# Kernel optimization log

Hardware: AMD Instinct MI355X
Metric: run time of the kernel (lower is better)

## Reference

```python
import jax, jax.numpy as jnp
import numpy as np

BLOCK = 128
QMAX = 127.0


def _quant_dequant_act(x2d):
    """Dynamic per-token, per-128-column-group INT8 quantize + dequantize.

    x2d: [T, K]. Groups of shape 1x128 along K (is_weight=False path).
    """
    T, K = x2d.shape
    xb = x2d.reshape(T, K // BLOCK, BLOCK)
    amax = jnp.max(jnp.abs(xb), axis=-1, keepdims=True)
    scale = jnp.where(amax > 0, amax / QMAX, 1.0)
    q = jnp.clip(jnp.round(xb / scale), -QMAX, QMAX)  # int8 values
    return (q * scale).reshape(T, K)


def _quant_dequant_weight(w):
    """128x128 blockwise INT8 quantize + dequantize (is_weight=True path).

    w: [O, K] with O, K multiples of 128.
    """
    O, K = w.shape
    wb = w.reshape(O // BLOCK, BLOCK, K // BLOCK, BLOCK)
    amax = jnp.max(jnp.abs(wb), axis=(1, 3), keepdims=True)
    scale = jnp.where(amax > 0, amax / QMAX, 1.0)
    q = jnp.clip(jnp.round(wb / scale), -QMAX, QMAX)
    return (q * scale).reshape(O, K)


def setup_inputs() -> dict:
    key = jax.random.key(0)
    k1, k2, k3 = jax.random.split(key, 3)
    B, S, K, O = 4, 2048, 4096, 11008
    x = jax.random.normal(k1, (B, S, K), dtype=jnp.float32)
    w = jax.random.normal(k2, (O, K), dtype=jnp.float32) * 0.02
    bias = jax.random.normal(k3, (O,), dtype=jnp.float32) * 0.01
    return {"x": x, "w": w, "bias": bias}


def reference(x, w, bias):
    """INT8Linear forward: dynamic per-token INT8 activation quantization +
    128x128 blockwise-scaled INT8 weight GEMM + bias.

    Because scales are constant within each (token-group x weight-block),
    the blockwise-scaled int8 GEMM is mathematically identical to
    dequantize-then-matmul, which is the efficient dense expression here.
    """
    in_shape = x.shape
    x2d = x.reshape(-1, in_shape[-1])        # [T, K]
    xdq = _quant_dequant_act(x2d)            # [T, K]
    wdq = _quant_dequant_weight(w)           # [O, K]
    y = jnp.einsum('tk,ok->to', xdq, wdq) + bias
    return y.reshape(*in_shape[:-1], w.shape[0])
```

## Files before the change

kernel.cpp:

```cpp
#include <hip/hip_runtime.h>
#include <hip/hip_bf16.h>
#include <stdint.h>

#define QMAXF 127.0f

typedef __attribute__((ext_vector_type(4))) float f32x4;
typedef __attribute__((ext_vector_type(4))) int i32x4;

typedef __attribute__((address_space(1))) void gbl_void;
typedef __attribute__((address_space(3))) void lds_void;

__device__ __forceinline__ void gload_lds16(const void* g, void* l) {
    __builtin_amdgcn_global_load_lds((const gbl_void*)g, (lds_void*)l, 16, 0, 0);
}

__global__ __launch_bounds__(256) void qd_x_kernel(const float* __restrict__ x,
                                                   char* __restrict__ qx,
                                                   float* __restrict__ sxT,
                                                   long ngroups, int nkb, int T) {
    long gw = ((long)blockIdx.x * blockDim.x + threadIdx.x) >> 6;
    int lane = threadIdx.x & 63;
    if (gw >= ngroups) return;

    float2 v = *(reinterpret_cast<const float2*>(x) + gw * 64 + lane);
    float a = fmaxf(fabsf(v.x), fabsf(v.y));
#pragma unroll
    for (int off = 32; off; off >>= 1) a = fmaxf(a, __shfl_xor(a, off));

    float scale = a > 0.f ? a / QMAXF : 1.f;
    int q0 = (int)fminf(fmaxf(rintf(v.x / scale), -QMAXF), QMAXF);
    int q1 = (int)fminf(fmaxf(rintf(v.y / scale), -QMAXF), QMAXF);
    unsigned short packed = (unsigned short)((q0 & 0xFF) | ((q1 & 0xFF) << 8));
    reinterpret_cast<unsigned short*>(qx)[gw * 64 + lane] = packed;

    if (lane == 0) {
        int t = (int)(gw / nkb), kb = (int)(gw - (long)t * nkb);
        sxT[(size_t)kb * T + t] = scale;
    }
}

__global__ __launch_bounds__(256) void qd_w_kernel(const float* __restrict__ w,
                                                   char* __restrict__ qw,
                                                   float* __restrict__ sw,
                                                   int K, int nkb) {
    int kb = blockIdx.x, ob = blockIdx.y;
    size_t base = (size_t)ob * 128 * K + (size_t)kb * 128;
    int t = threadIdx.x;

    float4 v[16];
    float a = 0.f;
#pragma unroll
    for (int i = 0; i < 16; i++) {
        int f = i * 256 + t;
        int row = f >> 5, c4 = f & 31;
        v[i] = *reinterpret_cast<const float4*>(w + base + (size_t)row * K + c4 * 4);
        a = fmaxf(a, fmaxf(fmaxf(fabsf(v[i].x), fabsf(v[i].y)),
                           fmaxf(fabsf(v[i].z), fabsf(v[i].w))));
    }
#pragma unroll
    for (int off = 32; off; off >>= 1) a = fmaxf(a, __shfl_xor(a, off));

    __shared__ float red[4];
    if ((t & 63) == 0) red[t >> 6] = a;
    __syncthreads();
    a = fmaxf(fmaxf(red[0], red[1]), fmaxf(red[2], red[3]));

    float scale = a > 0.f ? a / QMAXF : 1.f;
    if (t == 0) sw[(size_t)ob * nkb + kb] = scale;
#pragma unroll
    for (int i = 0; i < 16; i++) {
        int f = i * 256 + t;
        int row = f >> 5, c4 = f & 31;
        int q0 = (int)fminf(fmaxf(rintf(v[i].x / scale), -QMAXF), QMAXF);
        int q1 = (int)fminf(fmaxf(rintf(v[i].y / scale), -QMAXF), QMAXF);
        int q2 = (int)fminf(fmaxf(rintf(v[i].z / scale), -QMAXF), QMAXF);
        int q3 = (int)fminf(fmaxf(rintf(v[i].w / scale), -QMAXF), QMAXF);
        unsigned int p = (q0 & 0xFF) | ((q1 & 0xFF) << 8) | ((q2 & 0xFF) << 16) |
                         ((unsigned int)(q3 & 0xFF) << 24);
        *reinterpret_cast<unsigned int*>(qw + base + (size_t)row * K + c4 * 4) = p;
    }
}

#define GBM 256
#define GBN 256
#define SLOT_BY 65536

#define BAR()                              \
    do {                                   \
        asm volatile("" ::: "memory");     \
        __builtin_amdgcn_s_barrier();      \
        asm volatile("" ::: "memory");     \
    } while (0)
#define WAITL0()                                          \
    do {                                                  \
        asm volatile("s_waitcnt lgkmcnt(0)" ::: "memory");\
        __builtin_amdgcn_sched_barrier(0);                \
    } while (0)
#define WAITV0() asm volatile("s_waitcnt vmcnt(0)" ::: "memory")
#define SCHED0() __builtin_amdgcn_sched_barrier(0)

__global__ __launch_bounds__(512, 2) void gemm_i8_kernel(
    const char* __restrict__ Aq,
    const char* __restrict__ Bq,
    const float* __restrict__ sxT,
    const float* __restrict__ swp,
    const float* __restrict__ bias,
    float* __restrict__ C,
    int M, int N, int K) {
    __shared__ alignas(16) unsigned char lds8[2 * SLOT_BY];

    int nTm = M / GBM, nTn = N / GBN;
    int nwg = gridDim.x, wg = blockIdx.x;
    int mt, nt;
    if ((nTm & 7) == 0 && (32 % (nTm >> 3)) == 0) {
        int x = wg & 7, j = wg >> 3;
        int mper = nTm >> 3;
        int G = 32 / mper;
        int wsz = mper * G;
        int fullw = nTn / G;
        int jfull = fullw * wsz;
        int g, r, width;
        if (j < jfull) { g = j / wsz; r = j - g * wsz; width = G; }
        else { g = fullw; r = j - jfull; width = nTn - fullw * G; }
        mt = x * mper + r / width;
        nt = g * G + r % width;
    } else {
        int swz = (nwg & 7) ? wg : ((wg & 7) * (nwg >> 3) + (wg >> 3));
        mt = swz / nTn; nt = swz - mt * nTn;
    }

    int t = threadIdx.x, wid = t >> 6, lane = t & 63;
    int wm = wid >> 2, wn = wid & 3;
    int lr = lane & 15, lq = lane >> 4;
    int nkb = K >> 7;

    const char* Abase = Aq + (size_t)mt * GBM * K;
    const char* Bbase = Bq + (size_t)nt * GBN * K;

    int cid0 = t, cid1 = 512 + t;
    int rl0 = cid0 >> 3, rl1 = cid1 >> 3;
    int pc0 = cid0 & 7, pc1 = cid1 & 7;
    int gc0 = (pc0 ^ (rl0 & 7)) * 16, gc1 = (pc1 ^ (rl1 & 7)) * 16;

    auto STAGE = [&](int slot, int mat, int half, int kb) {
        const char* gb = (mat ? Bbase : Abase) + (size_t)(half * 128) * K + kb;
        unsigned char* db = lds8 + slot * SLOT_BY + mat * 32768 + half * 16384;
        gload_lds16(gb + (size_t)rl0 * K + gc0, db + cid0 * 16);
        gload_lds16(gb + (size_t)rl1 * K + gc1, db + cid1 * 16);
    };

    int offA[4][2], offB[2][2];
#pragma unroll
    for (int m = 0; m < 4; m++) {
        int row = wm * 128 + m * 16 + lr;
#pragma unroll
        for (int kk = 0; kk < 2; kk++)
            offA[m][kk] = row * 128 + (((kk * 4 + lq) ^ (lr & 7)) << 4);
    }
#pragma unroll
    for (int n = 0; n < 2; n++) {
        int row = wn * 64 + n * 16 + lr;
#pragma unroll
        for (int kk = 0; kk < 2; kk++)
            offB[n][kk] = 32768 + row * 128 + (((kk * 4 + lq) ^ (lr & 7)) << 4);
    }

    f32x4 facc[8][4];
#pragma unroll
    for (int m = 0; m < 8; m++)
#pragma unroll
        for (int n = 0; n < 4; n++) facc[m][n] = (f32x4){0.f, 0.f, 0.f, 0.f};

    i32x4 a[4][2], b[2][2], ia[4][2];

    auto LDA = [&](int slot, int mq) {
        const unsigned char* base = lds8 + slot * SLOT_BY + mq * 8192;
#pragma unroll
        for (int m = 0; m < 4; m++)
#pragma unroll
            for (int kk = 0; kk < 2; kk++)
                a[m][kk] = *reinterpret_cast<const i32x4*>(base + offA[m][kk]);
    };
    auto LDB = [&](int slot, int nq) {
        const unsigned char* base = lds8 + slot * SLOT_BY + nq * 4096;
#pragma unroll
        for (int n = 0; n < 2; n++)
#pragma unroll
            for (int kk = 0; kk < 2; kk++)
                b[n][kk] = *reinterpret_cast<const i32x4*>(base + offB[n][kk]);
    };
    auto MMA = [&]() {
        __builtin_amdgcn_s_setprio(1);
#pragma unroll
        for (int m = 0; m < 4; m++)
#pragma unroll
            for (int n = 0; n < 2; n++) {
                ia[m][n] = __builtin_amdgcn_mfma_i32_16x16x64_i8(
                    a[m][0], b[n][0], (i32x4){0, 0, 0, 0}, 0, 0, 0);
                ia[m][n] = __builtin_amdgcn_mfma_i32_16x16x64_i8(
                    a[m][1], b[n][1], ia[m][n], 0, 0, 0);
            }
        __builtin_amdgcn_s_setprio(0);
    };
    f32x4 sx4[4];
    float sw;
    auto FIX = [&](int mq, int nq) {
#pragma unroll
        for (int m = 0; m < 4; m++) {
            f32x4 sxw = sx4[m] * sw;
#pragma unroll
            for (int n = 0; n < 2; n++) {
                f32x4 cv;
#pragma unroll
                for (int r = 0; r < 4; r++) cv[r] = (float)ia[m][n][r];
                facc[mq * 4 + m][nq * 2 + n] += cv * sxw;
            }
        }
    };
    int sxrow0 = mt * GBM + wm * 128 + lq * 4;
    auto LDSX = [&](int i, int mq) {
#pragma unroll
        for (int m = 0; m < 4; m++)
            sx4[m] = *reinterpret_cast<const f32x4*>(
                sxT + (size_t)i * M + sxrow0 + mq * 64 + m * 16);
    };

    int swbase = (nt * 2 + (wn >> 1)) * nkb;

    STAGE(0, 0, 0, 0); STAGE(0, 0, 1, 0);
    STAGE(0, 1, 0, 0); STAGE(0, 1, 1, 0);
    WAITV0();
    BAR();

    for (int i = 0; i < nkb; ++i) {
        int p = i & 1, q = p ^ 1;
        int knext = (i + 1 < nkb ? i + 1 : i) * 128;

        LDA(p, 0); LDB(p, 0);
        STAGE(q, 0, 0, knext); STAGE(q, 1, 0, knext);
        LDSX(i, 0);
        sw = swp[swbase + i];
        BAR(); WAITL0();
        MMA(); FIX(0, 0);
        BAR();
        LDB(p, 1);
        STAGE(q, 0, 1, knext); STAGE(q, 1, 1, knext);
        BAR(); WAITL0();
        MMA(); FIX(0, 1);
        BAR();
        LDA(p, 1);
        LDSX(i, 1);
        BAR(); WAITL0();
        MMA(); FIX(1, 1);
        BAR();
        LDB(p, 0);
        BAR(); WAITL0();
        MMA(); FIX(1, 0);
        WAITV0();
        BAR();
    }

    float bvv[4];
#pragma unroll
    for (int n = 0; n < 4; n++) bvv[n] = bias[nt * GBN + wn * 64 + n * 16 + lr];

#pragma unroll
    for (int m = 0; m < 8; m++) {
#pragma unroll
        for (int r = 0; r < 4; r++) {
            size_t row = (size_t)(mt * GBM + wm * 128 + m * 16 + lq * 4 + r);
            float* Crow = C + row * N + nt * GBN + wn * 64 + lr;
#pragma unroll
            for (int n = 0; n < 4; n++) Crow[n * 16] = facc[m][n][r] + bvv[n];
        }
    }
}

extern "C" void kernel_launch(void* const* d_in, const int* in_sizes, int n_in,
                              void* d_out, int out_size, void* d_ws, size_t ws_size,
                              hipStream_t stream) {
    const float* x = (const float*)d_in[0];
    const float* w = (const float*)d_in[1];
    const float* bias = (const float*)d_in[2];
    float* y = (float*)d_out;

    int O = in_sizes[2];
    int K = in_sizes[1] / O;
    int T = in_sizes[0] / K;
    int nkb = K / 128;

    char* qx = (char*)d_ws;
    size_t off = ((size_t)T * K + 255) & ~(size_t)255;
    char* qw = (char*)d_ws + off;
    off += ((size_t)O * K + 255) & ~(size_t)255;
    float* sxT = (float*)((char*)d_ws + off);
    off += ((size_t)nkb * T * 4 + 255) & ~(size_t)255;
    float* sw = (float*)((char*)d_ws + off);

    long ngroups = (long)T * nkb;
    qd_x_kernel<<<dim3((unsigned)((ngroups + 3) / 4)), dim3(256), 0, stream>>>(
        x, qx, sxT, ngroups, nkb, T);
    qd_w_kernel<<<dim3(nkb, O / 128), dim3(256), 0, stream>>>(w, qw, sw, K, nkb);

    int grid = (T / GBM) * (O / GBN);
    gemm_i8_kernel<<<dim3(grid), dim3(512), 0, stream>>>(qx, qw, sxT, sw, bias, y,
                                                         T, O, K);
}
```

Measured before the change: 703.3 us.

## Restructure int8 GEMM main loop into 3-stage ring with 64-wide K sub-tiles

Replaces the double-buffered 128-K pipeline with a three-slot LDS ring of 64-K sub-tiles, prefetching two stages ahead with partial vmcnt waits so there is one barrier per sub-step instead of many. Activation scales are now staged into LDS alongside the tiles, and the weight scales are loaded once per wave and broadcast with a shuffle instead of being read from global memory every step. Occupancy drops from 2 to 1 workgroup per CU. The integer accumulators now cover only 64 of K before each float rescale, which doubles the convert and FMA fix-up work per MFMA.

Result: slower. 809.4 us (+15.1%).

```diff
diff --git a/kernel.cpp b/kernel.cpp
--- a/kernel.cpp
+++ b/kernel.cpp
@@ -83,7 +83,12 @@
 
 #define GBM 256
 #define GBN 256
-#define SLOT_BY 65536
+#define SUBK 64
+#define A_BY 16384
+#define B_BY 16384
+#define SX_BY 1024
+#define SLOT_BY (A_BY + B_BY + SX_BY)
+#define RING 3
 
 #define BAR()                              \
     do {                                   \
@@ -96,10 +101,9 @@
         asm volatile("s_waitcnt lgkmcnt(0)" ::: "memory");\
         __builtin_amdgcn_sched_barrier(0);                \
     } while (0)
-#define WAITV0() asm volatile("s_waitcnt vmcnt(0)" ::: "memory")
-#define SCHED0() __builtin_amdgcn_sched_barrier(0)
-
-__global__ __launch_bounds__(512, 2) void gemm_i8_kernel(
+#define WAITV(n) asm volatile("s_waitcnt vmcnt(" #n ")" ::: "memory")
+
+__global__ __launch_bounds__(512, 1) void gemm_i8_kernel(
     const char* __restrict__ Aq,
     const char* __restrict__ Bq,
     const float* __restrict__ sxT,
@@ -107,7 +111,7 @@
     const float* __restrict__ bias,
     float* __restrict__ C,
     int M, int N, int K) {
-    __shared__ alignas(16) unsigned char lds8[2 * SLOT_BY];
+    __shared__ alignas(16) unsigned char lds8[RING * SLOT_BY];
 
     int nTm = M / GBM, nTn = N / GBN;
     int nwg = gridDim.x, wg = blockIdx.x;
@@ -133,37 +137,44 @@
     int wm = wid >> 2, wn = wid & 3;
     int lr = lane & 15, lq = lane >> 4;
     int nkb = K >> 7;
+    int NSUB = K / SUBK;
 
     const char* Abase = Aq + (size_t)mt * GBM * K;
     const char* Bbase = Bq + (size_t)nt * GBN * K;
 
-    int cid0 = t, cid1 = 512 + t;
-    int rl0 = cid0 >> 3, rl1 = cid1 >> 3;
-    int pc0 = cid0 & 7, pc1 = cid1 & 7;
-    int gc0 = (pc0 ^ (rl0 & 7)) * 16, gc1 = (pc1 ^ (rl1 & 7)) * 16;
-
-    auto STAGE = [&](int slot, int mat, int half, int kb) {
-        const char* gb = (mat ? Bbase : Abase) + (size_t)(half * 128) * K + kb;
-        unsigned char* db = lds8 + slot * SLOT_BY + mat * 32768 + half * 16384;
-        gload_lds16(gb + (size_t)rl0 * K + gc0, db + cid0 * 16);
-        gload_lds16(gb + (size_t)rl1 * K + gc1, db + cid1 * 16);
+    {
+    }
+    int rA0 = t >> 2;
+    int pcc = t & 3;
+    int cA0 = (pcc ^ ((rA0 >> 1) & 3)) << 4;
+    const char* gA = Abase + (size_t)rA0 * K + cA0;
+    const char* gB = Bbase + (size_t)rA0 * K + cA0;
+    const char* gSX = (const char*)sxT + ((size_t)mt * GBM + (t & 63) * 4) * 4;
+    size_t rowStep = (size_t)128 * K;
+
+    auto STAGE = [&](int slot, int j) {
+        size_t kb = (size_t)j * SUBK;
+        unsigned char* sb = lds8 + slot * SLOT_BY;
+        gload_lds16(gA + kb, sb + t * 16);
+        gload_lds16(gA + rowStep + kb, sb + (512 + t) * 16);
+        gload_lds16(gB + kb, sb + A_BY + t * 16);
+        gload_lds16(gB + rowStep + kb, sb + A_BY + (512 + t) * 16);
+        gload_lds16(gSX + (size_t)(j >> 1) * M * 4, sb + A_BY + B_BY + (t & 63) * 16);
     };
 
-    int offA[4][2], offB[2][2];
-#pragma unroll
-    for (int m = 0; m < 4; m++) {
-        int row = wm * 128 + m * 16 + lr;
-#pragma unroll
-        for (int kk = 0; kk < 2; kk++)
-            offA[m][kk] = row * 128 + (((kk * 4 + lq) ^ (lr & 7)) << 4);
-    }
-#pragma unroll
-    for (int n = 0; n < 2; n++) {
-        int row = wn * 64 + n * 16 + lr;
-#pragma unroll
-        for (int kk = 0; kk < 2; kk++)
-            offB[n][kk] = 32768 + row * 128 + (((kk * 4 + lq) ^ (lr & 7)) << 4);
-    }
+    int physXor = (lq ^ ((lr >> 1) & 3)) << 4;
+    int offA[2][4], offB[4], offSX[2][4];
+#pragma unroll
+    for (int mq = 0; mq < 2; mq++)
+#pragma unroll
+        for (int m = 0; m < 4; m++) {
+            int row = wm * 128 + mq * 64 + m * 16;
+            offA[mq][m] = (row + lr) * 64 + physXor;
+            offSX[mq][m] = A_BY + B_BY + (row + lq * 4) * 4;
+        }
+#pragma unroll
+    for (int n = 0; n < 4; n++)
+        offB[n] = A_BY + (wn * 64 + n * 16 + lr) * 64 + physXor;
 
     f32x4 facc[8][4];
 #pragma unroll
@@ -171,94 +182,63 @@
 #pragma unroll
         for (int n = 0; n < 4; n++) facc[m][n] = (f32x4){0.f, 0.f, 0.f, 0.f};
 
-    i32x4 a[4][2], b[2][2], ia[4][2];
-
-    auto LDA = [&](int slot, int mq) {
-        const unsigned char* base = lds8 + slot * SLOT_BY + mq * 8192;
-#pragma unroll
-        for (int m = 0; m < 4; m++)
-#pragma unroll
-            for (int kk = 0; kk < 2; kk++)
-                a[m][kk] = *reinterpret_cast<const i32x4*>(base + offA[m][kk]);
-    };
-    auto LDB = [&](int slot, int nq) {
-        const unsigned char* base = lds8 + slot * SLOT_BY + nq * 4096;
-#pragma unroll
-        for (int n = 0; n < 2; n++)
-#pragma unroll
-            for (int kk = 0; kk < 2; kk++)
-                b[n][kk] = *reinterpret_cast<const i32x4*>(base + offB[n][kk]);
-    };
-    auto MMA = [&]() {
-        __builtin_amdgcn_s_setprio(1);
-#pragma unroll
-        for (int m = 0; m < 4; m++)
-#pragma unroll
-            for (int n = 0; n < 2; n++) {
-                ia[m][n] = __builtin_amdgcn_mfma_i32_16x16x64_i8(
-                    a[m][0], b[n][0], (i32x4){0, 0, 0, 0}, 0, 0, 0);
-                ia[m][n] = __builtin_amdgcn_mfma_i32_16x16x64_i8(
-                    a[m][1], b[n][1], ia[m][n], 0, 0, 0);
+    float swv = (lane < nkb) ? swp[(size_t)(nt * 2 + (wn >> 1)) * nkb + lane] : 0.f;
+
+    auto COMPUTE = [&](int slot, float swq) {
+        const unsigned char* sb = lds8 + slot * SLOT_BY;
+        i32x4 b[4];
+#pragma unroll
+        for (int n = 0; n < 4; n++)
+            b[n] = *reinterpret_cast<const i32x4*>(sb + offB[n]);
+#pragma unroll
+        for (int mq = 0; mq < 2; mq++) {
+            i32x4 a[4];
+            f32x4 sx4[4];
+#pragma unroll
+            for (int m = 0; m < 4; m++)
+                a[m] = *reinterpret_cast<const i32x4*>(sb + offA[mq][m]);
+#pragma unroll
+            for (int m = 0; m < 4; m++)
+                sx4[m] = *reinterpret_cast<const f32x4*>(sb + offSX[mq][m]);
+            WAITL0();
+            __builtin_amdgcn_s_setprio(1);
+#pragma unroll
+            for (int nq = 0; nq < 2; nq++) {
+                i32x4 ia[4][2];
+#pragma unroll
+                for (int m = 0; m < 4; m++)
+#pragma unroll
+                    for (int n2 = 0; n2 < 2; n2++)
+                        ia[m][n2] = __builtin_amdgcn_mfma_i32_16x16x64_i8(
+                            a[m], b[nq * 2 + n2], (i32x4){0, 0, 0, 0}, 0, 0, 0);
+#pragma unroll
+                for (int m = 0; m < 4; m++) {
+                    f32x4 s = sx4[m] * swq;
+#pragma unroll
+                    for (int n2 = 0; n2 < 2; n2++) {
+                        f32x4 cv;
+#pragma unroll
+                        for (int r = 0; r < 4; r++) cv[r] = (float)ia[m][n2][r];
+                        facc[mq * 4 + m][nq * 2 + n2] += cv * s;
+                    }
+                }
             }
-        __builtin_amdgcn_s_setprio(0);
-    };
-    f32x4 sx4[4];
-    float sw;
-    auto FIX = [&](int mq, int nq) {
-#pragma unroll
-        for (int m = 0; m < 4; m++) {
-            f32x4 sxw = sx4[m] * sw;
-#pragma unroll
-            for (int n = 0; n < 2; n++) {
-                f32x4 cv;
-#pragma unroll
-                for (int r = 0; r < 4; r++) cv[r] = (float)ia[m][n][r];
-                facc[mq * 4 + m][nq * 2 + n] += cv * sxw;
-            }
+            __builtin_amdgcn_s_setprio(0);
         }
     };
-    int sxrow0 = mt * GBM + wm * 128 + lq * 4;
-    auto LDSX = [&](int i, int mq) {
-#pragma unroll
-        for (int m = 0; m < 4; m++)
-            sx4[m] = *reinterpret_cast<const f32x4*>(
-                sxT + (size_t)i * M + sxrow0 + mq * 64 + m * 16);
-    };
-
-    int swbase = (nt * 2 + (wn >> 1)) * nkb;
-
-    STAGE(0, 0, 0, 0); STAGE(0, 0, 1, 0);
-    STAGE(0, 1, 0, 0); STAGE(0, 1, 1, 0);
-    WAITV0();
-    BAR();
-
-    for (int i = 0; i < nkb; ++i) {
-        int p = i & 1, q = p ^ 1;
-        int knext = (i + 1 < nkb ? i + 1 : i) * 128;
-
-        LDA(p, 0); LDB(p, 0);
-        STAGE(q, 0, 0, knext); STAGE(q, 1, 0, knext);
-        LDSX(i, 0);
-        sw = swp[swbase + i];
-        BAR(); WAITL0();
-        MMA(); FIX(0, 0);
+
+    STAGE(0, 0);
+    STAGE(1, 1);
+
+    for (int j = 0; j < NSUB; ++j) {
+        WAITV(5);
         BAR();
-        LDB(p, 1);
-        STAGE(q, 0, 1, knext); STAGE(q, 1, 1, knext);
-        BAR(); WAITL0();
-        MMA(); FIX(0, 1);
-        BAR();
-        LDA(p, 1);
-        LDSX(i, 1);
-        BAR(); WAITL0();
-        MMA(); FIX(1, 1);
-        BAR();
-        LDB(p, 0);
-        BAR(); WAITL0();
-        MMA(); FIX(1, 0);
-        WAITV0();
-        BAR();
-    }
+        int jn = j + 2 > NSUB - 1 ? NSUB - 1 : j + 2;
+        STAGE((j + 2) % RING, jn);
+        float swq = __shfl(swv, j >> 1);
+        COMPUTE(j % RING, swq);
+    }
+    asm volatile("s_waitcnt vmcnt(0)" ::: "memory");
 
     float bvv[4];
 #pragma unroll
```

## Restructure int8 GEMM main loop into two M-halves with fewer barriers

Applied to the files above, without the earlier changes.

The per-k-block loop moves from four quarter phases, each with its own barriers and partial LDS loads, to two M-half phases. Each phase loads all of B once and issues the full 4x4 MFMA set with the scale fix-up done inline. The next tile's global-to-LDS staging is issued at the top of the iteration, followed by targeted vmcnt waits and one barrier per iteration. Launch bounds drop to one workgroup per CU to allow more registers, so occupancy falls and latency hiding rests on the in-loop overlap.

After: 746.3 us. 1.06x slower.

```diff
diff --git a/kernel.cpp b/kernel.cpp
--- a/kernel.cpp
+++ b/kernel.cpp
@@ -96,10 +96,10 @@
         asm volatile("s_waitcnt lgkmcnt(0)" ::: "memory");\
         __builtin_amdgcn_sched_barrier(0);                \
     } while (0)
-#define WAITV0() asm volatile("s_waitcnt vmcnt(0)" ::: "memory")
+#define WAITV(n) asm volatile("s_waitcnt vmcnt(" #n ")" ::: "memory")
 #define SCHED0() __builtin_amdgcn_sched_barrier(0)
 
-__global__ __launch_bounds__(512, 2) void gemm_i8_kernel(
+__global__ __launch_bounds__(512, 1) void gemm_i8_kernel(
     const char* __restrict__ Aq,
     const char* __restrict__ Bq,
     const float* __restrict__ sxT,
@@ -109,12 +109,12 @@
     int M, int N, int K) {
     __shared__ alignas(16) unsigned char lds8[2 * SLOT_BY];
 
-    int nTm = M / GBM, nTn = N / GBN;
+    int nTm = M >> 8, nTn = N >> 8;
     int nwg = gridDim.x, wg = blockIdx.x;
     int mt, nt;
-    if ((nTm & 7) == 0 && (32 % (nTm >> 3)) == 0) {
+    int mper = nTm >> 3;
+    if ((nTm & 7) == 0 && mper > 0 && (32 % mper) == 0) {
         int x = wg & 7, j = wg >> 3;
-        int mper = nTm >> 3;
         int G = 32 / mper;
         int wsz = mper * G;
         int fullw = nTn / G;
@@ -139,17 +139,24 @@
 
     int cid0 = t, cid1 = 512 + t;
     int rl0 = cid0 >> 3, rl1 = cid1 >> 3;
-    int pc0 = cid0 & 7, pc1 = cid1 & 7;
-    int gc0 = (pc0 ^ (rl0 & 7)) * 16, gc1 = (pc1 ^ (rl1 & 7)) * 16;
-
-    auto STAGE = [&](int slot, int mat, int half, int kb) {
-        const char* gb = (mat ? Bbase : Abase) + (size_t)(half * 128) * K + kb;
-        unsigned char* db = lds8 + slot * SLOT_BY + mat * 32768 + half * 16384;
-        gload_lds16(gb + (size_t)rl0 * K + gc0, db + cid0 * 16);
-        gload_lds16(gb + (size_t)rl1 * K + gc1, db + cid1 * 16);
-    };
-
-    int offA[4][2], offB[2][2];
+    int gc0 = ((cid0 & 7) ^ (rl0 & 7)) * 16, gc1 = ((cid1 & 7) ^ (rl1 & 7)) * 16;
+
+    auto STAGE8 = [&](int slot, int kb) {
+        unsigned char* sb = lds8 + slot * SLOT_BY;
+#pragma unroll
+        for (int half = 0; half < 2; half++) {
+            const char* ga = Abase + (size_t)(half * 128) * K + kb;
+            const char* gb = Bbase + (size_t)(half * 128) * K + kb;
+            unsigned char* da = sb + half * 16384;
+            unsigned char* db = sb + 32768 + half * 16384;
+            gload_lds16(ga + (size_t)rl0 * K + gc0, da + cid0 * 16);
+            gload_lds16(ga + (size_t)rl1 * K + gc1, da + cid1 * 16);
+            gload_lds16(gb + (size_t)rl0 * K + gc0, db + cid0 * 16);
+            gload_lds16(gb + (size_t)rl1 * K + gc1, db + cid1 * 16);
+        }
+    };
+
+    int offA[4][2], offB[4][2];
 #pragma unroll
     for (int m = 0; m < 4; m++) {
         int row = wm * 128 + m * 16 + lr;
@@ -158,7 +165,7 @@
             offA[m][kk] = row * 128 + (((kk * 4 + lq) ^ (lr & 7)) << 4);
     }
 #pragma unroll
-    for (int n = 0; n < 2; n++) {
+    for (int n = 0; n < 4; n++) {
         int row = wn * 64 + n * 16 + lr;
 #pragma unroll
         for (int kk = 0; kk < 2; kk++)
@@ -171,7 +178,9 @@
 #pragma unroll
         for (int n = 0; n < 4; n++) facc[m][n] = (f32x4){0.f, 0.f, 0.f, 0.f};
 
-    i32x4 a[4][2], b[2][2], ia[4][2];
+    i32x4 aH[4][2], b[4][2];
+    f32x4 sx4[4];
+    float swq = 0.f;
 
     auto LDA = [&](int slot, int mq) {
         const unsigned char* base = lds8 + slot * SLOT_BY + mq * 8192;
@@ -179,43 +188,15 @@
         for (int m = 0; m < 4; m++)
 #pragma unroll
             for (int kk = 0; kk < 2; kk++)
-                a[m][kk] = *reinterpret_cast<const i32x4*>(base + offA[m][kk]);
-    };
-    auto LDB = [&](int slot, int nq) {
-        const unsigned char* base = lds8 + slot * SLOT_BY + nq * 4096;
-#pragma unroll
-        for (int n = 0; n < 2; n++)
+                aH[m][kk] = *reinterpret_cast<const i32x4*>(base + offA[m][kk]);
+    };
+    auto LDB = [&](int slot) {
+        const unsigned char* base = lds8 + slot * SLOT_BY;
+#pragma unroll
+        for (int n = 0; n < 4; n++)
 #pragma unroll
             for (int kk = 0; kk < 2; kk++)
                 b[n][kk] = *reinterpret_cast<const i32x4*>(base + offB[n][kk]);
-    };
-    auto MMA = [&]() {
-        __builtin_amdgcn_s_setprio(1);
-#pragma unroll
-        for (int m = 0; m < 4; m++)
-#pragma unroll
-            for (int n = 0; n < 2; n++) {
-                ia[m][n] = __builtin_amdgcn_mfma_i32_16x16x64_i8(
-                    a[m][0], b[n][0], (i32x4){0, 0, 0, 0}, 0, 0, 0);
-                ia[m][n] = __builtin_amdgcn_mfma_i32_16x16x64_i8(
-                    a[m][1], b[n][1], ia[m][n], 0, 0, 0);
-            }
-        __builtin_amdgcn_s_setprio(0);
-    };
-    f32x4 sx4[4];
-    float sw;
-    auto FIX = [&](int mq, int nq) {
-#pragma unroll
-        for (int m = 0; m < 4; m++) {
-            f32x4 sxw = sx4[m] * sw;
-#pragma unroll
-            for (int n = 0; n < 2; n++) {
-                f32x4 cv;
-#pragma unroll
-                for (int r = 0; r < 4; r++) cv[r] = (float)ia[m][n][r];
-                facc[mq * 4 + m][nq * 2 + n] += cv * sxw;
-            }
-        }
     };
     int sxrow0 = mt * GBM + wm * 128 + lq * 4;
     auto LDSX = [&](int i, int mq) {
@@ -224,39 +205,54 @@
             sx4[m] = *reinterpret_cast<const f32x4*>(
                 sxT + (size_t)i * M + sxrow0 + mq * 64 + m * 16);
     };
+    auto MQ = [&](int mq) {
+        __builtin_amdgcn_s_setprio(1);
+#pragma unroll
+        for (int m = 0; m < 4; m++) {
+            i32x4 ia[4];
+#pragma unroll
+            for (int n = 0; n < 4; n++) {
+                ia[n] = __builtin_amdgcn_mfma_i32_16x16x64_i8(aH[m][0], b[n][0],
+                                                              (i32x4){0, 0, 0, 0}, 0, 0, 0);
+                ia[n] = __builtin_amdgcn_mfma_i32_16x16x64_i8(aH[m][1], b[n][1],
+                                                              ia[n], 0, 0, 0);
+            }
+            f32x4 s = sx4[m] * swq;
+#pragma unroll
+            for (int n = 0; n < 4; n++) {
+#pragma unroll
+                for (int r = 0; r < 4; r++)
+                    facc[mq * 4 + m][n][r] += (float)ia[n][r] * s[r];
+            }
+        }
+        __builtin_amdgcn_s_setprio(0);
+    };
 
     int swbase = (nt * 2 + (wn >> 1)) * nkb;
 
-    STAGE(0, 0, 0, 0); STAGE(0, 0, 1, 0);
-    STAGE(0, 1, 0, 0); STAGE(0, 1, 1, 0);
-    WAITV0();
+    STAGE8(0, 0);
+    WAITV(0);
     BAR();
 
     for (int i = 0; i < nkb; ++i) {
         int p = i & 1, q = p ^ 1;
         int knext = (i + 1 < nkb ? i + 1 : i) * 128;
 
-        LDA(p, 0); LDB(p, 0);
-        STAGE(q, 0, 0, knext); STAGE(q, 1, 0, knext);
         LDSX(i, 0);
-        sw = swp[swbase + i];
-        BAR(); WAITL0();
-        MMA(); FIX(0, 0);
-        BAR();
-        LDB(p, 1);
-        STAGE(q, 0, 1, knext); STAGE(q, 1, 1, knext);
-        BAR(); WAITL0();
-        MMA(); FIX(0, 1);
-        BAR();
+        swq = swp[swbase + i];
+        SCHED0();
+        STAGE8(q, knext);
+        SCHED0();
+        LDA(p, 0);
+        LDB(p);
+        WAITL0();
+        WAITV(8);
+        MQ(0);
         LDA(p, 1);
         LDSX(i, 1);
-        BAR(); WAITL0();
-        MMA(); FIX(1, 1);
-        BAR();
-        LDB(p, 0);
-        BAR(); WAITL0();
-        MMA(); FIX(1, 0);
-        WAITV0();
+        WAITL0();
+        WAITV(0);
+        MQ(1);
         BAR();
     }
 
@@ -302,7 +298,7 @@
         x, qx, sxT, ngroups, nkb, T);
     qd_w_kernel<<<dim3(nkb, O / 128), dim3(256), 0, stream>>>(w, qw, sw, K, nkb);
 
-    int grid = (T / GBM) * (O / GBN);
+    int grid = (T / 256) * (O / 256);
     gemm_i8_kernel<<<dim3(grid), dim3(512), 0, stream>>>(qx, qw, sxT, sw, bias, y,
                                                          T, O, K);
 }
```
